# Optimization experiments

Measured on AMD Instinct MI355X. Metric: run time of the kernel, lower is better.

Reference implementation:

```python
import jax, jax.numpy as jnp
import numpy as np
import math

B, S, D_MODEL, N_HEAD = 4, 2048, 1024, 16
D_K = D_MODEL // N_HEAD
ROPE_THETA = 10000.0


def _rope(x):
    # x: [B, H, S, Dk]; interleaved-pair rotary embedding.
    b, h, s, d = x.shape
    inv_freq = ROPE_THETA ** (-jnp.arange(0, d, 2, dtype=jnp.float32) / d)  # [d/2]
    ang = jnp.arange(s, dtype=jnp.float32)[:, None] * inv_freq[None, :]      # [S, d/2]
    cos, sin = jnp.cos(ang), jnp.sin(ang)
    x1, x2 = x[..., 0::2], x[..., 1::2]
    r1 = x1 * cos - x2 * sin
    r2 = x1 * sin + x2 * cos
    return jnp.stack([r1, r2], axis=-1).reshape(b, h, s, d)


def setup_inputs() -> dict:
    key = jax.random.key(0)
    ks = jax.random.split(key, 7)
    sc = 1.0 / math.sqrt(D_MODEL)
    return {
        "q": jax.random.normal(ks[0], (B, S, D_MODEL), jnp.float32),
        "k": jax.random.normal(ks[1], (B, S, D_MODEL), jnp.float32),
        "v": jax.random.normal(ks[2], (B, S, D_MODEL), jnp.float32),
        "Wq": jax.random.normal(ks[3], (D_MODEL, D_MODEL), jnp.float32) * sc,
        "Wk": jax.random.normal(ks[4], (D_MODEL, D_MODEL), jnp.float32) * sc,
        "Wv": jax.random.normal(ks[5], (D_MODEL, D_MODEL), jnp.float32) * sc,
        "Wo": jax.random.normal(ks[6], (D_MODEL, D_MODEL), jnp.float32) * sc,
    }


def _split(x):
    b, s, d = x.shape
    return x.reshape(b, s, N_HEAD, d // N_HEAD).transpose(0, 2, 1, 3)  # [B,H,S,Dk]


def reference(q, k, v, Wq, Wk, Wv, Wo):
    q = jnp.einsum("bsd,de->bse", q, Wq)
    k = jnp.einsum("bsd,de->bse", k, Wk)
    v = jnp.einsum("bsd,de->bse", v, Wv)
    qh, kh, vh = _split(q), _split(k), _split(v)
    qh, kh = _rope(qh), _rope(kh)
    scale = 1.0 / math.sqrt(D_K)
    score = jnp.einsum("bhqd,bhkd->bhqk", qh, kh) * scale  # [B,H,S,S]
    attn = jax.nn.softmax(score, axis=-1)
    out = jnp.einsum("bhqk,bhkd->bhqd", attn, vh)
    out = out.transpose(0, 2, 1, 3).reshape(q.shape[0], q.shape[1], D_MODEL)
    return jnp.einsum("bsd,de->bse", out, Wo)
```

## Files before the change

### kernel.cpp

```cpp
#include <hip/hip_runtime.h>
#include <stdint.h>

#define Bv 4
#define Sv 2048
#define Dv 1024
#define Hv 16
#define DKv 64
#define BSv (Bv * Sv)

typedef unsigned short u16;
typedef __attribute__((ext_vector_type(8))) short short8;
typedef __attribute__((ext_vector_type(8))) unsigned short u16x8;
typedef __attribute__((ext_vector_type(4))) unsigned short u16x4;
typedef __attribute__((ext_vector_type(4))) float f32x4;
typedef __attribute__((ext_vector_type(16))) float f32x16;

__device__ __forceinline__ u16 f2bf(float f) {
  union { float f; uint32_t u; } x; x.f = f;
  uint32_t r = x.u + 0x7FFFu + ((x.u >> 16) & 1u);
  return (u16)(r >> 16);
}

__device__ __forceinline__ void gl_lds16(const void* g, void* l) {
  __builtin_amdgcn_global_load_lds(
      (__attribute__((address_space(1))) void*)g,
      (__attribute__((address_space(3))) void*)l, 16, 0, 0);
}

__device__ __forceinline__ f32x4 mfma16(short8 a, short8 b, f32x4 c) {
  return __builtin_amdgcn_mfma_f32_16x16x32_bf16(a, b, c, 0, 0, 0);
}
__device__ __forceinline__ f32x16 mfma32(short8 a, short8 b, f32x16 c) {
  return __builtin_amdgcn_mfma_f32_32x32x16_bf16(a, b, c, 0, 0, 0);
}

template <int N>
__device__ __forceinline__ void vwait() {
  asm volatile("s_waitcnt vmcnt(%0)" ::"n"(N) : "memory");
}
__device__ __forceinline__ void bar() {
  asm volatile("" ::: "memory");
  __builtin_amdgcn_s_barrier();
  asm volatile("" ::: "memory");
}

__global__ __launch_bounds__(256) void conv_qkv(
    const float* __restrict__ q, const float* __restrict__ k,
    const float* __restrict__ v, u16* __restrict__ qb, u16* __restrict__ kb,
    u16* __restrict__ vb) {
  const float* src = (blockIdx.y == 0) ? q : (blockIdx.y == 1 ? k : v);
  u16* dst = (blockIdx.y == 0) ? qb : (blockIdx.y == 1 ? kb : vb);
  int i = (blockIdx.x * 256 + threadIdx.x) * 8;
  const float4* s4 = (const float4*)(src + i);
  float4 a = s4[0], b = s4[1];
  u16x8 o = { f2bf(a.x), f2bf(a.y), f2bf(a.z), f2bf(a.w),
              f2bf(b.x), f2bf(b.y), f2bf(b.z), f2bf(b.w) };
  *(u16x8*)(dst + i) = o;
}

__global__ __launch_bounds__(256) void conv_wt(
    const float* __restrict__ w0, const float* __restrict__ w1,
    const float* __restrict__ w2, const float* __restrict__ w3,
    u16* __restrict__ t0, u16* __restrict__ t1, u16* __restrict__ t2,
    u16* __restrict__ t3) {
  const float* W = (blockIdx.z == 0) ? w0 : (blockIdx.z == 1 ? w1 : (blockIdx.z == 2 ? w2 : w3));
  u16* T = (blockIdx.z == 0) ? t0 : (blockIdx.z == 1 ? t1 : (blockIdx.z == 2 ? t2 : t3));
  __shared__ u16 tile[64][72];
  int nb = blockIdx.x * 64, kb = blockIdx.y * 64;
  int t = threadIdx.x;
#pragma unroll
  for (int p = 0; p < 4; ++p) {
    int idx = p * 256 + t;
    int r = idx >> 4;
    int c4 = (idx & 15) * 4;
    float4 vv = *(const float4*)(W + (size_t)(kb + r) * Dv + nb + c4);
    tile[c4 + 0][r] = f2bf(vv.x);
    tile[c4 + 1][r] = f2bf(vv.y);
    tile[c4 + 2][r] = f2bf(vv.z);
    tile[c4 + 3][r] = f2bf(vv.w);
  }
  __syncthreads();
#pragma unroll
  for (int p = 0; p < 4; ++p) {
    int idx = p * 256 + t;
    int r = idx >> 4;
    int c4 = (idx & 15) * 4;
    u16x4 o = { tile[r][c4], tile[r][c4 + 1], tile[r][c4 + 2], tile[r][c4 + 3] };
    *(u16x4*)(T + (size_t)(nb + r) * Dv + kb + c4) = o;
  }
}

__global__ __launch_bounds__(512, 2) void gemm_bt(
    const u16* __restrict__ A0, const u16* __restrict__ A1, const u16* __restrict__ A2,
    const u16* __restrict__ B0, const u16* __restrict__ B1, const u16* __restrict__ B2,
    void* __restrict__ O0, void* __restrict__ O1, void* __restrict__ O2,
    int modeSel) {
  __shared__ u16 As[3][256 * 64];
  __shared__ u16 Bs[3][128 * 64];
  int z = blockIdx.z;
  const u16* A  = (z == 0) ? A0 : (z == 1 ? A1 : A2);
  const u16* Bt = (z == 0) ? B0 : (z == 1 ? B1 : B2);
  void* Out     = (z == 0) ? O0 : (z == 1 ? O1 : O2);
  int mode = (modeSel < 0) ? z : modeSel;

  int tid = threadIdx.x;
  int lane = tid & 63, wid = tid >> 6;
  int quad = lane >> 4, cc = lane & 15;
  int wm = (wid >> 1) * 64, wn = (wid & 1) * 64;
  int bx = blockIdx.x;
  int swz = (bx & 7) * 32 + (bx >> 3);
  int m0 = (swz >> 3) * 256, n0 = (swz & 7) * 128;

  f32x4 acc[4][4];
#pragma unroll
  for (int mi = 0; mi < 4; ++mi)
#pragma unroll
    for (int ni = 0; ni < 4; ++ni) {
      f32x4 zf = {0.f, 0.f, 0.f, 0.f};
      acc[mi][ni] = zf;
    }

  auto stageA2 = [&](int ki, int b, int p0) {
#pragma unroll
    for (int p = 0; p < 2; ++p) {
      int slot = (p0 + p) * 512 + tid;
      int row = slot >> 3, cl = slot & 7;
      int cg = cl ^ (row & 7);
      gl_lds16(A + (size_t)(m0 + row) * Dv + ki * 64 + cg * 8, &As[b][slot * 8]);
    }
  };
  auto stageB1 = [&](int ki, int b, int p0) {
    int slot = p0 * 512 + tid;
    int row = slot >> 3, cl = slot & 7;
    int cg = cl ^ (row & 7);
    gl_lds16(Bt + (size_t)(n0 + row) * Dv + ki * 64 + cg * 8, &Bs[b][slot * 8]);
  };

  stageA2(0, 0, 0); stageA2(0, 0, 2); stageB1(0, 0, 0); stageB1(0, 0, 1);
  stageA2(1, 1, 0); stageA2(1, 1, 2); stageB1(1, 1, 0); stageB1(1, 1, 1);
  vwait<6>();
  bar();

  const int NT = Dv / 64;
  int cur = 0, nxt = 2;
#pragma unroll 1
  for (int t = 0; t < NT; ++t) {
    const u16* Ac = &As[cur][0];
    const u16* Bc = &Bs[cur][0];
#pragma unroll
    for (int kk = 0; kk < 2; ++kk) {
      short8 af[4], bfr[4];
#pragma unroll
      for (int mi = 0; mi < 4; ++mi) {
        int row = wm + mi * 16 + cc;
        int cg = kk * 4 + quad;
        af[mi] = *(const short8*)&Ac[row * 64 + (cg ^ (row & 7)) * 8];
      }
#pragma unroll
      for (int ni = 0; ni < 4; ++ni) {
        int row = wn + ni * 16 + cc;
        int cg = kk * 4 + quad;
        bfr[ni] = *(const short8*)&Bc[row * 64 + (cg ^ (row & 7)) * 8];
      }
      if (t + 2 < NT) {
        if (kk == 0) { stageA2(t + 2, nxt, 0); stageB1(t + 2, nxt, 0); }
        else         { stageA2(t + 2, nxt, 2); stageB1(t + 2, nxt, 1); }
      }
      bar();
      __builtin_amdgcn_s_setprio(1);
#pragma unroll
      for (int mi = 0; mi < 4; ++mi)
#pragma unroll
        for (int ni = 0; ni < 4; ++ni)
          acc[mi][ni] = mfma16(af[mi], bfr[ni], acc[mi][ni]);
      __builtin_amdgcn_s_setprio(0);
      if (kk == 0) bar();
    }
    if (t < NT - 1) {
      if (t + 2 < NT) vwait<6>(); else vwait<0>();
      bar();
    }
    cur = (cur == 2) ? 0 : cur + 1;
    nxt = (nxt == 2) ? 0 : nxt + 1;
  }

  if (mode <= 1) {
    u16* O = (u16*)Out;
    float postscale = (mode == 0) ? 0.18033688011112042f : 1.0f;
#pragma unroll
    for (int ni = 0; ni < 4; ++ni) {
      int n = n0 + wn + ni * 16 + cc;
      int h = n >> 6, d = n & 63;
      float inv = __expf(-(float)(d & 62) * (9.210340372f / 64.0f));
      float sign = (d & 1) ? 1.0f : -1.0f;
#pragma unroll
      for (int mi = 0; mi < 4; ++mi) {
        int mB = m0 + wm + mi * 16 + quad * 4;
#pragma unroll
        for (int r = 0; r < 4; ++r) {
          int m = mB + r;
          int b = m >> 11, s = m & (Sv - 1);
          float val = acc[mi][ni][r];
          float part = __shfl_xor(val, 1);
          float sn, cs;
          __sincosf((float)s * inv, &sn, &cs);
          float outv = (val * cs + sign * part * sn) * postscale;
          O[((size_t)(b * Hv + h) * Sv + s) * DKv + d] = f2bf(outv);
        }
      }
    }
  } else if (mode == 2) {
    u16* O = (u16*)Out;
#pragma unroll
    for (int ni = 0; ni < 4; ++ni) {
      int n = n0 + wn + ni * 16 + cc;
      int h = n >> 6, d = n & 63;
#pragma unroll
      for (int mi = 0; mi < 4; ++mi) {
        int mB = m0 + wm + mi * 16 + quad * 4;
        int b = mB >> 11, s = mB & (Sv - 1);
        u16x4 o4 = { f2bf(acc[mi][ni][0]), f2bf(acc[mi][ni][1]),
                     f2bf(acc[mi][ni][2]), f2bf(acc[mi][ni][3]) };
        *(u16x4*)&O[((size_t)(b * Hv + h) * DKv + d) * Sv + s] = o4;
      }
    }
  } else {
    float* O = (float*)Out;
#pragma unroll
    for (int ni = 0; ni < 4; ++ni) {
      int n = n0 + wn + ni * 16 + cc;
#pragma unroll
      for (int mi = 0; mi < 4; ++mi) {
        int mB = m0 + wm + mi * 16 + quad * 4;
#pragma unroll
        for (int r = 0; r < 4; ++r)
          O[(size_t)(mB + r) * Dv + n] = acc[mi][ni][r];
      }
    }
  }
}

__global__ __launch_bounds__(256, 2) void attn(
    const u16* __restrict__ Qp, const u16* __restrict__ Kp,
    const u16* __restrict__ Vt, u16* __restrict__ ctx) {
  __shared__ u16 Ks[2][64 * 64];
  __shared__ u16 Vs[2][64 * 64];
  int tid = threadIdx.x;
  int lane = tid & 63, wid = tid >> 6;
  int hi = lane >> 5, c32 = lane & 31;
  int sz = (c32 & 7) ^ ((c32 >> 3) & 3);
  int bh = blockIdx.y;
  int q0 = blockIdx.x * 256 + wid * 64;
  const u16* Qh = Qp + (size_t)bh * Sv * DKv;
  const u16* Kh = Kp + (size_t)bh * Sv * DKv;
  const u16* Vh = Vt + (size_t)bh * Sv * DKv;

  const short8 ones = { (short)0x3F80, (short)0x3F80, (short)0x3F80, (short)0x3F80,
                        (short)0x3F80, (short)0x3F80, (short)0x3F80, (short)0x3F80 };

  short8 qf[2][4];
#pragma unroll
  for (int qs = 0; qs < 2; ++qs)
#pragma unroll
    for (int dk = 0; dk < 4; ++dk)
      qf[qs][dk] = *(const short8*)&Qh[(size_t)(q0 + qs * 32 + c32) * DKv + dk * 16 + hi * 8];

  f32x16 o[2][2];
  f32x16 ol[2];
#pragma unroll
  for (int qs = 0; qs < 2; ++qs) {
#pragma unroll
    for (int dt = 0; dt < 2; ++dt)
#pragma unroll
      for (int r = 0; r < 16; ++r) o[qs][dt][r] = 0.f;
#pragma unroll
    for (int r = 0; r < 16; ++r) ol[qs][r] = 0.f;
  }

#pragma unroll
  for (int p = 0; p < 2; ++p) {
    int slot = p * 256 + tid;
    int row = slot >> 3, cl = slot & 7;
    int cg = cl ^ ((row & 7) ^ ((row >> 3) & 3));
    gl_lds16(Kh + (size_t)row * DKv + cg * 8, &Ks[0][slot * 8]);
    gl_lds16(Vh + (size_t)row * Sv + cg * 8, &Vs[0][slot * 8]);
  }

  for (int kt = 0; kt < Sv / 64; ++kt) {
    int cur = kt & 1;
    __syncthreads();

    if (kt + 1 < Sv / 64) {
      int s1 = (kt + 1) * 64;
#pragma unroll
      for (int p = 0; p < 2; ++p) {
        int slot = p * 256 + tid;
        int row = slot >> 3, cl = slot & 7;
        int cg = cl ^ ((row & 7) ^ ((row >> 3) & 3));
        gl_lds16(Kh + (size_t)(s1 + row) * DKv + cg * 8, &Ks[1 - cur][slot * 8]);
        gl_lds16(Vh + (size_t)row * Sv + s1 + cg * 8, &Vs[1 - cur][slot * 8]);
      }
    }

#pragma unroll
    for (int half = 0; half < 2; ++half) {
      short8 kf[4];
#pragma unroll
      for (int dk = 0; dk < 4; ++dk)
        kf[dk] = *(const short8*)&Ks[cur][(half * 32 + c32) * 64 + (((dk * 2 + hi) ^ sz)) * 8];

      f32x16 st[2];
#pragma unroll
      for (int qs = 0; qs < 2; ++qs) {
#pragma unroll
        for (int r = 0; r < 16; ++r) st[qs][r] = 0.f;
#pragma unroll
        for (int dk = 0; dk < 4; ++dk)
          st[qs] = mfma32(kf[dk], qf[qs][dk], st[qs]);
      }

#pragma unroll
      for (int pp = 0; pp < 2; ++pp) {
        int pk = half * 2 + pp;
        short8 vf[2];
#pragma unroll
        for (int dt = 0; dt < 2; ++dt)
          vf[dt] = *(const short8*)&Vs[cur][(dt * 32 + c32) * 64 + (((pk * 2 + hi) ^ sz)) * 8];
#pragma unroll
        for (int qs = 0; qs < 2; ++qs) {
          float e0 = __builtin_amdgcn_exp2f(st[qs][8 * pp + 0]);
          float e1 = __builtin_amdgcn_exp2f(st[qs][8 * pp + 1]);
          float e2 = __builtin_amdgcn_exp2f(st[qs][8 * pp + 2]);
          float e3 = __builtin_amdgcn_exp2f(st[qs][8 * pp + 3]);
          float e4 = __builtin_amdgcn_exp2f(st[qs][8 * pp + 4]);
          float e5 = __builtin_amdgcn_exp2f(st[qs][8 * pp + 5]);
          float e6 = __builtin_amdgcn_exp2f(st[qs][8 * pp + 6]);
          float e7 = __builtin_amdgcn_exp2f(st[qs][8 * pp + 7]);
          uint32_t plo0 = __builtin_amdgcn_perm(__float_as_uint(e1), __float_as_uint(e0), 0x07060302u);
          uint32_t plo1 = __builtin_amdgcn_perm(__float_as_uint(e3), __float_as_uint(e2), 0x07060302u);
          uint32_t phi0 = __builtin_amdgcn_perm(__float_as_uint(e5), __float_as_uint(e4), 0x07060302u);
          uint32_t phi1 = __builtin_amdgcn_perm(__float_as_uint(e7), __float_as_uint(e6), 0x07060302u);
          uint32_t s0 = hi ? plo0 : phi0;
          uint32_t s1 = hi ? plo1 : phi1;
          uint32_t r0 = (uint32_t)__shfl_xor((int)s0, 32);
          uint32_t r1 = (uint32_t)__shfl_xor((int)s1, 32);
          union { uint32_t u[4]; short8 s8; } pu;
          pu.u[0] = hi ? r0 : plo0;
          pu.u[1] = hi ? r1 : plo1;
          pu.u[2] = hi ? phi0 : r0;
          pu.u[3] = hi ? phi1 : r1;
          ol[qs] = mfma32(pu.s8, ones, ol[qs]);
          o[qs][0] = mfma32(pu.s8, vf[0], o[qs][0]);
          o[qs][1] = mfma32(pu.s8, vf[1], o[qs][1]);
        }
      }
    }
  }

  int b = bh >> 4, h = bh & 15;
#pragma unroll
  for (int qs = 0; qs < 2; ++qs)
#pragma unroll
    for (int r = 0; r < 16; ++r) {
      int q = q0 + qs * 32 + (r & 3) + 8 * (r >> 2) + 4 * hi;
      float linv = 1.0f / ol[qs][r];
#pragma unroll
      for (int dt = 0; dt < 2; ++dt) {
        int d = h * DKv + dt * 32 + c32;
        ctx[((size_t)b * Sv + q) * Dv + d] = f2bf(o[qs][dt][r] * linv);
      }
    }
}

extern "C" void kernel_launch(void* const* d_in, const int* in_sizes, int n_in,
                              void* d_out, int out_size, void* d_ws, size_t ws_size,
                              hipStream_t stream) {
  (void)in_sizes; (void)n_in; (void)out_size; (void)ws_size;
  const float* q  = (const float*)d_in[0];
  const float* k  = (const float*)d_in[1];
  const float* v  = (const float*)d_in[2];
  const float* Wq = (const float*)d_in[3];
  const float* Wk = (const float*)d_in[4];
  const float* Wv = (const float*)d_in[5];
  const float* Wo = (const float*)d_in[6];

  char* ws = (char*)d_ws;
  size_t off = 0;
  const size_t big = (size_t)BSv * Dv * sizeof(u16);
  const size_t wsz = (size_t)Dv * Dv * sizeof(u16);
  u16* qb  = (u16*)(ws + off); off += big;
  u16* kb  = (u16*)(ws + off); off += big;
  u16* vb  = (u16*)(ws + off); off += big;
  u16* Wqt = (u16*)(ws + off); off += wsz;
  u16* Wkt = (u16*)(ws + off); off += wsz;
  u16* Wvt = (u16*)(ws + off); off += wsz;
  u16* Wot = (u16*)(ws + off); off += wsz;
  u16* Qp  = (u16*)(ws + off); off += big;
  u16* Kp  = (u16*)(ws + off); off += big;
  u16* Vtr = (u16*)(ws + off); off += big;
  u16* ctx = (u16*)(ws + off); off += big;

  conv_qkv<<<dim3(BSv * Dv / (256 * 8), 3), 256, 0, stream>>>(q, k, v, qb, kb, vb);
  conv_wt<<<dim3(Dv / 64, Dv / 64, 4), 256, 0, stream>>>(Wq, Wk, Wv, Wo, Wqt, Wkt, Wvt, Wot);
  gemm_bt<<<dim3(256, 1, 3), 512, 0, stream>>>(
      qb, kb, vb, Wqt, Wkt, Wvt, Qp, Kp, Vtr, -1);
  attn<<<dim3(Sv / 256, Bv * Hv), 256, 0, stream>>>(Qp, Kp, Vtr, ctx);
  gemm_bt<<<dim3(256, 1, 1), 512, 0, stream>>>(
      ctx, ctx, ctx, Wot, Wot, Wot, d_out, d_out, d_out, 3);
}
```

Before: 327.7 us.

## Fuse fp32-to-bf16 input conversion into QKV GEMM and reshape attention grid

Drops the separate conv_qkv pass. A new gemm_qkv kernel loads fp32 activations directly, converts them to bf16 in registers and writes them to LDS, while RoPE and scale epilogues stay in the kernel. This removes a full read/write of three bf16 activation copies. The attention kernel now gives each wave 32 queries instead of 64 and raises the occupancy hint to 4, with a swizzled 1D grid that interleaves heads. The cost is more K/V LDS traffic per query and register-staged A loads in the GEMM.

Measured after the change: 343.6 us. 1.05x slower.

```diff
diff --git a/kernel.cpp b/kernel.cpp
--- a/kernel.cpp
+++ b/kernel.cpp
@@ -42,20 +42,6 @@
   asm volatile("" ::: "memory");
   __builtin_amdgcn_s_barrier();
   asm volatile("" ::: "memory");
-}
-
-__global__ __launch_bounds__(256) void conv_qkv(
-    const float* __restrict__ q, const float* __restrict__ k,
-    const float* __restrict__ v, u16* __restrict__ qb, u16* __restrict__ kb,
-    u16* __restrict__ vb) {
-  const float* src = (blockIdx.y == 0) ? q : (blockIdx.y == 1 ? k : v);
-  u16* dst = (blockIdx.y == 0) ? qb : (blockIdx.y == 1 ? kb : vb);
-  int i = (blockIdx.x * 256 + threadIdx.x) * 8;
-  const float4* s4 = (const float4*)(src + i);
-  float4 a = s4[0], b = s4[1];
-  u16x8 o = { f2bf(a.x), f2bf(a.y), f2bf(a.z), f2bf(a.w),
-              f2bf(b.x), f2bf(b.y), f2bf(b.z), f2bf(b.w) };
-  *(u16x8*)(dst + i) = o;
 }
 
 __global__ __launch_bounds__(256) void conv_wt(
@@ -87,6 +73,143 @@
     int c4 = (idx & 15) * 4;
     u16x4 o = { tile[r][c4], tile[r][c4 + 1], tile[r][c4 + 2], tile[r][c4 + 3] };
     *(u16x4*)(T + (size_t)(nb + r) * Dv + kb + c4) = o;
+  }
+}
+
+__global__ __launch_bounds__(256, 2) void gemm_qkv(
+    const float* __restrict__ A0, const float* __restrict__ A1, const float* __restrict__ A2,
+    const u16* __restrict__ B0, const u16* __restrict__ B1, const u16* __restrict__ B2,
+    u16* __restrict__ O0, u16* __restrict__ O1, u16* __restrict__ O2) {
+  __shared__ u16 As[2][128 * 64];
+  __shared__ u16 Bs[2][128 * 64];
+  int z = blockIdx.z;
+  const float* A = (z == 0) ? A0 : (z == 1 ? A1 : A2);
+  const u16* Bt  = (z == 0) ? B0 : (z == 1 ? B1 : B2);
+  u16* Out       = (z == 0) ? O0 : (z == 1 ? O1 : O2);
+  int mode = z;
+
+  int tid = threadIdx.x;
+  int lane = tid & 63, wid = tid >> 6;
+  int quad = lane >> 4, cc = lane & 15;
+  int wm = (wid >> 1) * 64, wn = (wid & 1) * 64;
+  int m0 = blockIdx.x * 128, n0 = blockIdx.y * 128;
+
+  f32x4 acc[4][4];
+#pragma unroll
+  for (int mi = 0; mi < 4; ++mi)
+#pragma unroll
+    for (int ni = 0; ni < 4; ++ni) {
+      f32x4 zf = {0.f, 0.f, 0.f, 0.f};
+      acc[mi][ni] = zf;
+    }
+
+  auto stageB = [&](int ki, int b) {
+#pragma unroll
+    for (int p = 0; p < 4; ++p) {
+      int slot = p * 256 + tid;
+      int row = slot >> 3, cl = slot & 7;
+      int cg = cl ^ (row & 7);
+      gl_lds16(Bt + (size_t)(n0 + row) * Dv + ki * 64 + cg * 8, &Bs[b][slot * 8]);
+    }
+  };
+
+  float4 fa[4][2];
+  auto loadA = [&](int ki) {
+#pragma unroll
+    for (int p = 0; p < 4; ++p) {
+      int slot = p * 256 + tid;
+      int row = slot >> 3, cl = slot & 7;
+      int cg = cl ^ (row & 7);
+      const float* g = A + (size_t)(m0 + row) * Dv + ki * 64 + cg * 8;
+      fa[p][0] = *(const float4*)g;
+      fa[p][1] = *(const float4*)(g + 4);
+    }
+  };
+  auto writeA = [&](int b) {
+#pragma unroll
+    for (int p = 0; p < 4; ++p) {
+      int slot = p * 256 + tid;
+      u16x8 o = { f2bf(fa[p][0].x), f2bf(fa[p][0].y), f2bf(fa[p][0].z), f2bf(fa[p][0].w),
+                  f2bf(fa[p][1].x), f2bf(fa[p][1].y), f2bf(fa[p][1].z), f2bf(fa[p][1].w) };
+      *(u16x8*)&As[b][slot * 8] = o;
+    }
+  };
+
+  loadA(0); writeA(0); stageB(0, 0);
+
+  const int NT = Dv / 64;
+  for (int t = 0; t < NT; ++t) {
+    int cur = t & 1;
+    __syncthreads();
+
+    if (t + 1 < NT) {
+      stageB(t + 1, 1 - cur);
+      loadA(t + 1);
+    }
+
+#pragma unroll
+    for (int kk = 0; kk < 2; ++kk) {
+      short8 af[4], bfr[4];
+#pragma unroll
+      for (int mi = 0; mi < 4; ++mi) {
+        int row = wm + mi * 16 + cc;
+        int cg = kk * 4 + quad;
+        af[mi] = *(const short8*)&As[cur][row * 64 + (cg ^ (row & 7)) * 8];
+      }
+#pragma unroll
+      for (int ni = 0; ni < 4; ++ni) {
+        int row = wn + ni * 16 + cc;
+        int cg = kk * 4 + quad;
+        bfr[ni] = *(const short8*)&Bs[cur][row * 64 + (cg ^ (row & 7)) * 8];
+      }
+#pragma unroll
+      for (int mi = 0; mi < 4; ++mi)
+#pragma unroll
+        for (int ni = 0; ni < 4; ++ni)
+          acc[mi][ni] = mfma16(af[mi], bfr[ni], acc[mi][ni]);
+    }
+
+    if (t + 1 < NT) writeA(1 - cur);
+  }
+
+  if (mode <= 1) {
+    float postscale = (mode == 0) ? 0.18033688011112042f : 1.0f;
+#pragma unroll
+    for (int ni = 0; ni < 4; ++ni) {
+      int n = n0 + wn + ni * 16 + cc;
+      int h = n >> 6, d = n & 63;
+      float inv = __expf(-(float)(d & 62) * (9.210340372f / 64.0f));
+      float sign = (d & 1) ? 1.0f : -1.0f;
+#pragma unroll
+      for (int mi = 0; mi < 4; ++mi) {
+        int mB = m0 + wm + mi * 16 + quad * 4;
+#pragma unroll
+        for (int r = 0; r < 4; ++r) {
+          int m = mB + r;
+          int b = m >> 11, s = m & (Sv - 1);
+          float val = acc[mi][ni][r];
+          float part = __shfl_xor(val, 1);
+          float sn, cs;
+          __sincosf((float)s * inv, &sn, &cs);
+          float outv = (val * cs + sign * part * sn) * postscale;
+          Out[((size_t)(b * Hv + h) * Sv + s) * DKv + d] = f2bf(outv);
+        }
+      }
+    }
+  } else {
+#pragma unroll
+    for (int ni = 0; ni < 4; ++ni) {
+      int n = n0 + wn + ni * 16 + cc;
+      int h = n >> 6, d = n & 63;
+#pragma unroll
+      for (int mi = 0; mi < 4; ++mi) {
+        int mB = m0 + wm + mi * 16 + quad * 4;
+        int b = mB >> 11, s = mB & (Sv - 1);
+        u16x4 o4 = { f2bf(acc[mi][ni][0]), f2bf(acc[mi][ni][1]),
+                     f2bf(acc[mi][ni][2]), f2bf(acc[mi][ni][3]) };
+        *(u16x4*)&Out[((size_t)(b * Hv + h) * DKv + d) * Sv + s] = o4;
+      }
+    }
   }
 }
 
@@ -240,7 +363,7 @@
   }
 }
 
-__global__ __launch_bounds__(256, 2) void attn(
+__global__ __launch_bounds__(256, 4) void attn(
     const u16* __restrict__ Qp, const u16* __restrict__ Kp,
     const u16* __restrict__ Vt, u16* __restrict__ ctx) {
   __shared__ u16 Ks[2][64 * 64];
@@ -249,8 +372,10 @@
   int lane = tid & 63, wid = tid >> 6;
   int hi = lane >> 5, c32 = lane & 31;
   int sz = (c32 & 7) ^ ((c32 >> 3) & 3);
-  int bh = blockIdx.y;
-  int q0 = blockIdx.x * 256 + wid * 64;
+  int bx = blockIdx.x;
+  int u = (bx & 7) * 128 + (bx >> 3);
+  int bh = u >> 4;
+  int q0 = (u & 15) * 128 + wid * 32;
   const u16* Qh = Qp + (size_t)bh * Sv * DKv;
   const u16* Kh = Kp + (size_t)bh * Sv * DKv;
   const u16* Vh = Vt + (size_t)bh * Sv * DKv;
@@ -258,24 +383,19 @@
   const short8 ones = { (short)0x3F80, (short)0x3F80, (short)0x3F80, (short)0x3F80,
                         (short)0x3F80, (short)0x3F80, (short)0x3F80, (short)0x3F80 };
 
-  short8 qf[2][4];
-#pragma unroll
-  for (int qs = 0; qs < 2; ++qs)
-#pragma unroll
-    for (int dk = 0; dk < 4; ++dk)
-      qf[qs][dk] = *(const short8*)&Qh[(size_t)(q0 + qs * 32 + c32) * DKv + dk * 16 + hi * 8];
-
-  f32x16 o[2][2];
-  f32x16 ol[2];
-#pragma unroll
-  for (int qs = 0; qs < 2; ++qs) {
-#pragma unroll
-    for (int dt = 0; dt < 2; ++dt)
-#pragma unroll
-      for (int r = 0; r < 16; ++r) o[qs][dt][r] = 0.f;
-#pragma unroll
-    for (int r = 0; r < 16; ++r) ol[qs][r] = 0.f;
-  }
+  short8 qf[4];
+#pragma unroll
+  for (int dk = 0; dk < 4; ++dk)
+    qf[dk] = *(const short8*)&Qh[(size_t)(q0 + c32) * DKv + dk * 16 + hi * 8];
+
+  f32x16 o[2];
+  f32x16 ol;
+#pragma unroll
+  for (int dt = 0; dt < 2; ++dt)
+#pragma unroll
+    for (int r = 0; r < 16; ++r) o[dt][r] = 0.f;
+#pragma unroll
+  for (int r = 0; r < 16; ++r) ol[r] = 0.f;
 
 #pragma unroll
   for (int p = 0; p < 2; ++p) {
@@ -309,15 +429,12 @@
       for (int dk = 0; dk < 4; ++dk)
         kf[dk] = *(const short8*)&Ks[cur][(half * 32 + c32) * 64 + (((dk * 2 + hi) ^ sz)) * 8];
 
-      f32x16 st[2];
-#pragma unroll
-      for (int qs = 0; qs < 2; ++qs) {
-#pragma unroll
-        for (int r = 0; r < 16; ++r) st[qs][r] = 0.f;
-#pragma unroll
-        for (int dk = 0; dk < 4; ++dk)
-          st[qs] = mfma32(kf[dk], qf[qs][dk], st[qs]);
-      }
+      f32x16 st;
+#pragma unroll
+      for (int r = 0; r < 16; ++r) st[r] = 0.f;
+#pragma unroll
+      for (int dk = 0; dk < 4; ++dk)
+        st = mfma32(kf[dk], qf[dk], st);
 
 #pragma unroll
       for (int pp = 0; pp < 2; ++pp) {
@@ -326,50 +443,45 @@
 #pragma unroll
         for (int dt = 0; dt < 2; ++dt)
           vf[dt] = *(const short8*)&Vs[cur][(dt * 32 + c32) * 64 + (((pk * 2 + hi) ^ sz)) * 8];
-#pragma unroll
-        for (int qs = 0; qs < 2; ++qs) {
-          float e0 = __builtin_amdgcn_exp2f(st[qs][8 * pp + 0]);
-          float e1 = __builtin_amdgcn_exp2f(st[qs][8 * pp + 1]);
-          float e2 = __builtin_amdgcn_exp2f(st[qs][8 * pp + 2]);
-          float e3 = __builtin_amdgcn_exp2f(st[qs][8 * pp + 3]);
-          float e4 = __builtin_amdgcn_exp2f(st[qs][8 * pp + 4]);
-          float e5 = __builtin_amdgcn_exp2f(st[qs][8 * pp + 5]);
-          float e6 = __builtin_amdgcn_exp2f(st[qs][8 * pp + 6]);
-          float e7 = __builtin_amdgcn_exp2f(st[qs][8 * pp + 7]);
-          uint32_t plo0 = __builtin_amdgcn_perm(__float_as_uint(e1), __float_as_uint(e0), 0x07060302u);
-          uint32_t plo1 = __builtin_amdgcn_perm(__float_as_uint(e3), __float_as_uint(e2), 0x07060302u);
-          uint32_t phi0 = __builtin_amdgcn_perm(__float_as_uint(e5), __float_as_uint(e4), 0x07060302u);
-          uint32_t phi1 = __builtin_amdgcn_perm(__float_as_uint(e7), __float_as_uint(e6), 0x07060302u);
-          uint32_t s0 = hi ? plo0 : phi0;
-          uint32_t s1 = hi ? plo1 : phi1;
-          uint32_t r0 = (uint32_t)__shfl_xor((int)s0, 32);
-          uint32_t r1 = (uint32_t)__shfl_xor((int)s1, 32);
-          union { uint32_t u[4]; short8 s8; } pu;
-          pu.u[0] = hi ? r0 : plo0;
-          pu.u[1] = hi ? r1 : plo1;
-          pu.u[2] = hi ? phi0 : r0;
-          pu.u[3] = hi ? phi1 : r1;
-          ol[qs] = mfma32(pu.s8, ones, ol[qs]);
-          o[qs][0] = mfma32(pu.s8, vf[0], o[qs][0]);
-          o[qs][1] = mfma32(pu.s8, vf[1], o[qs][1]);
-        }
+        float e0 = __builtin_amdgcn_exp2f(st[8 * pp + 0]);
+        float e1 = __builtin_amdgcn_exp2f(st[8 * pp + 1]);
+        float e2 = __builtin_amdgcn_exp2f(st[8 * pp + 2]);
+        float e3 = __builtin_amdgcn_exp2f(st[8 * pp + 3]);
+        float e4 = __builtin_amdgcn_exp2f(st[8 * pp + 4]);
+        float e5 = __builtin_amdgcn_exp2f(st[8 * pp + 5]);
+        float e6 = __builtin_amdgcn_exp2f(st[8 * pp + 6]);
+        float e7 = __builtin_amdgcn_exp2f(st[8 * pp + 7]);
+        uint32_t plo0 = __builtin_amdgcn_perm(__float_as_uint(e1), __float_as_uint(e0), 0x07060302u);
+        uint32_t plo1 = __builtin_amdgcn_perm(__float_as_uint(e3), __float_as_uint(e2), 0x07060302u);
+        uint32_t phi0 = __builtin_amdgcn_perm(__float_as_uint(e5), __float_as_uint(e4), 0x07060302u);
+        uint32_t phi1 = __builtin_amdgcn_perm(__float_as_uint(e7), __float_as_uint(e6), 0x07060302u);
+        uint32_t s0 = hi ? plo0 : phi0;
+        uint32_t s1 = hi ? plo1 : phi1;
+        uint32_t r0 = (uint32_t)__shfl_xor((int)s0, 32);
+        uint32_t r1 = (uint32_t)__shfl_xor((int)s1, 32);
+        union { uint32_t u[4]; short8 s8; } pu;
+        pu.u[0] = hi ? r0 : plo0;
+        pu.u[1] = hi ? r1 : plo1;
+        pu.u[2] = hi ? phi0 : r0;
+        pu.u[3] = hi ? phi1 : r1;
+        ol = mfma32(pu.s8, ones, ol);
+        o[0] = mfma32(pu.s8, vf[0], o[0]);
+        o[1] = mfma32(pu.s8, vf[1], o[1]);
       }
     }
   }
 
   int b = bh >> 4, h = bh & 15;
 #pragma unroll
-  for (int qs = 0; qs < 2; ++qs)
-#pragma unroll
-    for (int r = 0; r < 16; ++r) {
-      int q = q0 + qs * 32 + (r & 3) + 8 * (r >> 2) + 4 * hi;
-      float linv = 1.0f / ol[qs][r];
-#pragma unroll
-      for (int dt = 0; dt < 2; ++dt) {
-        int d = h * DKv + dt * 32 + c32;
-        ctx[((size_t)b * Sv + q) * Dv + d] = f2bf(o[qs][dt][r] * linv);
-      }
-    }
+  for (int r = 0; r < 16; ++r) {
+    int q = q0 + (r & 3) + 8 * (r >> 2) + 4 * hi;
+    float linv = 1.0f / ol[r];
+#pragma unroll
+    for (int dt = 0; dt < 2; ++dt) {
+      int d = h * DKv + dt * 32 + c32;
+      ctx[((size_t)b * Sv + q) * Dv + d] = f2bf(o[dt][r] * linv);
+    }
+  }
 }
 
 extern "C" void kernel_launch(void* const* d_in, const int* in_sizes, int n_in,
@@ -388,9 +500,6 @@
   size_t off = 0;
   const size_t big = (size_t)BSv * Dv * sizeof(u16);
   const size_t wsz = (size_t)Dv * Dv * sizeof(u16);
-  u16* qb  = (u16*)(ws + off); off += big;
-  u16* kb  = (u16*)(ws + off); off += big;
-  u16* vb  = (u16*)(ws + off); off += big;
   u16* Wqt = (u16*)(ws + off); off += wsz;
   u16* Wkt = (u16*)(ws + off); off += wsz;
   u16* Wvt = (u16*)(ws + off); off += wsz;
@@ -400,11 +509,10 @@
   u16* Vtr = (u16*)(ws + off); off += big;
   u16* ctx = (u16*)(ws + off); off += big;
 
-  conv_qkv<<<dim3(BSv * Dv / (256 * 8), 3), 256, 0, stream>>>(q, k, v, qb, kb, vb);
   conv_wt<<<dim3(Dv / 64, Dv / 64, 4), 256, 0, stream>>>(Wq, Wk, Wv, Wo, Wqt, Wkt, Wvt, Wot);
-  gemm_bt<<<dim3(256, 1, 3), 512, 0, stream>>>(
-      qb, kb, vb, Wqt, Wkt, Wvt, Qp, Kp, Vtr, -1);
-  attn<<<dim3(Sv / 256, Bv * Hv), 256, 0, stream>>>(Qp, Kp, Vtr, ctx);
+  gemm_qkv<<<dim3(BSv / 128, Dv / 128, 3), 256, 0, stream>>>(
+      q, k, v, Wqt, Wkt, Wvt, Qp, Kp, Vtr);
+  attn<<<dim3(Sv / 128 * Bv * Hv), 256, 0, stream>>>(Qp, Kp, Vtr, ctx);
   gemm_bt<<<dim3(256, 1, 1), 512, 0, stream>>>(
       ctx, ctx, ctx, Wot, Wot, Wot, d_out, d_out, d_out, 3);
 }
```
